# Performance work log

Measured on AMD Instinct MI355X. Metric: run time of the kernel, lower is better.

## Reference

```python
import jax, jax.numpy as jnp
import numpy as np

DIM = 1024
NUM_HEADS = 16
HEAD_DIM = DIM // NUM_HEADS
SCALE = HEAD_DIM ** -0.5


def setup_inputs() -> dict:
    key = jax.random.key(0)
    k1, k2, k3, k4, k5 = jax.random.split(key, 5)
    B, N = 2, 2048
    h = jax.random.normal(k1, (B, N, DIM), dtype=jnp.float32)
    mask = jax.random.uniform(k2, (B, N), dtype=jnp.float32)  # non-negative, sqrt-safe
    # nn.Linear(dim, dim*3, bias=False): weight applied as x @ W^T; store as [dim, 3*dim]
    w_qkv = jax.random.normal(k3, (DIM, 3 * DIM), dtype=jnp.float32) * (DIM ** -0.5)
    w_proj = jax.random.normal(k4, (DIM, DIM), dtype=jnp.float32) * (DIM ** -0.5)
    b_proj = jax.random.normal(k5, (DIM,), dtype=jnp.float32) * 0.01
    return {"h": h, "mask": mask, "w_qkv": w_qkv, "w_proj": w_proj, "b_proj": b_proj}


def reference(h, mask, w_qkv, w_proj, b_proj):
    B, N, C = h.shape
    H, D = NUM_HEADS, HEAD_DIM
    # qkv projection -> [3, B, H, N, D]
    qkv = (h @ w_qkv).reshape(B, N, 3, H, D).transpose(2, 0, 3, 1, 4)
    q, k, v = qkv[0], qkv[1], qkv[2]
    # scores [B,H,N,N]; scale applied to logits (same math as (q@k^T)*scale)
    attn = jax.nn.softmax(jnp.einsum('bhqd,bhkd->bhqk', q, k) * SCALE, axis=-1)
    # post-softmax multiplicative mask over the KEY dimension: mask[B,N]->[B,1,1,N]
    attn = attn * mask[:, None, None, :]
    new_mask = jnp.sqrt(mask)
    out = jnp.einsum('bhqk,bhkd->bhqd', attn, v)          # [B,H,N,D]
    out = out.transpose(0, 2, 1, 3).reshape(B, N, C)       # [B,N,C]
    out = out @ w_proj + b_proj
    return out, new_mask
```

## Files before the change

kernel.cpp:

```cpp
#include <hip/hip_runtime.h>
#include <hip/hip_bf16.h>
#include <math.h>

#define DIMC   1024
#define NHEADS 16
#define HDIM   64
#define BATCH  2
#define SEQ    2048
#define SCALE  0.125f
#define QSCL   (0.125f * 1.44269504088896341f)

typedef unsigned short u16;
typedef unsigned int   u32;
typedef __attribute__((ext_vector_type(8))) short bf16x8;
typedef _Float16 f16x8 __attribute__((ext_vector_type(8)));
typedef __attribute__((ext_vector_type(4))) float f32x4;

#define BHND ((size_t)BATCH * NHEADS * SEQ * HDIM)
#define MROWS ((size_t)BATCH * SEQ)

__device__ __forceinline__ u16 f2bf(float x) {
    __hip_bfloat16 h = __float2bfloat16(x);
    return *reinterpret_cast<u16*>(&h);
}
__device__ __forceinline__ u16 f2h(float x) {
    _Float16 h = (_Float16)x;
    return *reinterpret_cast<u16*>(&h);
}
__device__ __forceinline__ u32 cvt_pk_bf16(float a, float b) {
    u32 r;
    asm("v_cvt_pk_bf16_f32 %0, %1, %2" : "=v"(r) : "v"(a), "v"(b));
    return r;
}
__device__ __forceinline__ void gload_lds16(const u16* g, u16* l) {
    __builtin_amdgcn_global_load_lds(
        (const __attribute__((address_space(1))) unsigned int*)g,
        (__attribute__((address_space(3))) unsigned int*)l, 16, 0, 0);
}

__global__ __launch_bounds__(256) void prep_h_kernel(
    const float* __restrict__ in, u16* __restrict__ outh,
    const float* __restrict__ mask, float* __restrict__ outm)
{
    int bid = blockIdx.x;
    if (bid < 2048) {
        int i = (bid * 256 + threadIdx.x) * 8;
        float4 a = *(const float4*)&in[i];
        float4 b = *(const float4*)&in[i + 4];
        float v[8] = {a.x, a.y, a.z, a.w, b.x, b.y, b.z, b.w};
        bf16x8 o;
        #pragma unroll
        for (int j = 0; j < 8; ++j) o[j] = (short)f2h(v[j]);
        *(bf16x8*)&outh[i] = o;
    } else {
        int i = ((bid - 2048) * 256 + threadIdx.x) * 8;
        float4 a = *(const float4*)&mask[i];
        float4 b = *(const float4*)&mask[i + 4];
        float4 oa = make_float4(sqrtf(a.x), sqrtf(a.y), sqrtf(a.z), sqrtf(a.w));
        float4 ob = make_float4(sqrtf(b.x), sqrtf(b.y), sqrtf(b.z), sqrtf(b.w));
        *(float4*)&outm[i]     = oa;
        *(float4*)&outm[i + 4] = ob;
    }
}

__global__ __launch_bounds__(256) void prep_w_kernel(
    const float* __restrict__ Wq, const float* __restrict__ Wp,
    u16* __restrict__ Tq, u16* __restrict__ Tp)
{
    __shared__ float Ws[64][65];
    const int K = DIMC;
    const float* W; u16* T; int N, nb;
    if (blockIdx.y < 48) { W = Wq; T = Tq; N = 3072; nb = blockIdx.y * 64; }
    else                 { W = Wp; T = Tp; N = 1024; nb = (blockIdx.y - 48) * 64; }
    const int kb  = blockIdx.x * 64;
    const int tid = threadIdx.x;
    const int jr  = (tid & 15) * 4;
    const int ir  = tid >> 4;
    #pragma unroll
    for (int it = 0; it < 4; ++it) {
        int i = ir + it * 16;
        *(float4*)&Ws[i][jr] = *(const float4*)&W[(size_t)(kb + i) * N + nb + jr];
    }
    __syncthreads();
    const int n  = tid >> 2;
    const int k0 = (tid & 3) * 16;
    bf16x8 h0, h1;
    #pragma unroll
    for (int kk = 0; kk < 8; ++kk) {
        h0[kk] = (short)f2h(Ws[k0 + kk][n]);
        h1[kk] = (short)f2h(Ws[k0 + 8 + kk][n]);
    }
    size_t off = (size_t)(nb + n) * K + kb + k0;
    *(bf16x8*)&T[off]     = h0;
    *(bf16x8*)&T[off + 8] = h1;
}

template <int MODE>
__global__ __launch_bounds__(256) void gemm_f16_kernel(
    const u16* __restrict__ A, const u16* __restrict__ B,
    const float* __restrict__ bias, const float* __restrict__ vmask,
    float* __restrict__ outf, u16* __restrict__ outb,
    int M, int N, int K)
{
    __shared__ __align__(16) u16 lds[2][128 * 64];

    const int bm   = blockIdx.y * 128;
    const int bn   = blockIdx.x * 128;
    const int tid  = threadIdx.x;
    const int wid  = tid >> 6;
    const int lane = tid & 63;
    const int lo   = lane & 15;
    const int g4   = lane >> 4;
    const int wr   = wid >> 1, wc = wid & 1;

    const int srow8 = lane >> 3;
    const int scolx = 8 * ((lane & 7) ^ srow8);
    const u16* g0  = (wid < 2)
        ? A + (size_t)(bm + (wid & 1) * 64 + srow8) * K + scolx
        : B + (size_t)(bn + (wid & 1) * 64 + srow8) * K + scolx;
    u16* lbase = &lds[wid >> 1][(wid & 1) * 64 * 64];

    f32x4 acc[4][4] = {};

    for (int k0 = 0; k0 < K; k0 += 64) {
        const u16* g = g0 + k0;
        #pragma unroll
        for (int s = 0; s < 8; ++s)
            gload_lds16(g + (size_t)s * 8 * K, lbase + s * 512);
        __syncthreads();

        #pragma unroll
        for (int ks = 0; ks < 2; ++ks) {
            const int csw = 8 * ((4 * ks + g4) ^ (lo & 7));
            f16x8 bfr[4];
            #pragma unroll
            for (int ni = 0; ni < 4; ++ni)
                bfr[ni] = *(const f16x8*)&lds[1][(wc * 64 + ni * 16 + lo) * 64 + csw];
            #pragma unroll
            for (int mi = 0; mi < 4; ++mi) {
                f16x8 a = *(const f16x8*)&lds[0][(wr * 64 + mi * 16 + lo) * 64 + csw];
                #pragma unroll
                for (int ni = 0; ni < 4; ++ni)
                    acc[mi][ni] = __builtin_amdgcn_mfma_f32_16x16x32_f16(a, bfr[ni], acc[mi][ni], 0, 0, 0);
            }
        }
        __syncthreads();
    }

    if (MODE == 0) {
        #pragma unroll
        for (int mi = 0; mi < 4; ++mi) {
            int m0 = bm + wr * 64 + mi * 16 + 4 * g4;
            #pragma unroll
            for (int ni = 0; ni < 4; ++ni) {
                int n0    = bn + wc * 64 + ni * 16;
                int which = n0 >> 10;
                int head  = (n0 & 1023) >> 6;
                int d     = (n0 & 63) + lo;
                if (which == 0) {
                    #pragma unroll
                    for (int r = 0; r < 4; ++r) {
                        int m = m0 + r, b = m >> 11, seq = m & 2047;
                        outb[(((size_t)b * NHEADS + head) * SEQ + seq) * HDIM + d] =
                            f2bf(acc[mi][ni][r] * QSCL);
                    }
                } else if (which == 1) {
                    #pragma unroll
                    for (int r = 0; r < 4; ++r) {
                        int m = m0 + r, b = m >> 11, seq = m & 2047;
                        outb[BHND + (((size_t)b * NHEADS + head) * SEQ + seq) * HDIM + d] =
                            f2bf(acc[mi][ni][r]);
                    }
                } else {
                    int b = m0 >> 11, seq0 = m0 & 2047;
                    float4 mv = *(const float4*)&vmask[b * SEQ + seq0];
                    ushort4 o;
                    o.x = f2bf(acc[mi][ni][0] * mv.x);
                    o.y = f2bf(acc[mi][ni][1] * mv.y);
                    o.z = f2bf(acc[mi][ni][2] * mv.z);
                    o.w = f2bf(acc[mi][ni][3] * mv.w);
                    *(ushort4*)&outb[2 * BHND +
                        (((size_t)b * NHEADS + head) * HDIM + d) * SEQ + seq0] = o;
                }
            }
        }
    } else {
        #pragma unroll
        for (int ni = 0; ni < 4; ++ni) {
            int col = bn + wc * 64 + ni * 16 + lo;
            float bv = bias[col];
            #pragma unroll
            for (int mi = 0; mi < 4; ++mi) {
                int m0 = bm + wr * 64 + mi * 16 + 4 * g4;
                #pragma unroll
                for (int r = 0; r < 4; ++r)
                    outf[(size_t)(m0 + r) * N + col] = acc[mi][ni][r] + bv;
            }
        }
    }
}

__global__ __launch_bounds__(256) void attn_mfma_kernel(
    const u16* __restrict__ qb, const u16* __restrict__ kb,
    const u16* __restrict__ vtb, u16* __restrict__ oA)
{
    __shared__ __align__(16) u16 Ks[64 * 64];
    __shared__ __align__(16) u16 Vt[64 * 64];
    __shared__ __align__(16) u16 Plds[4][16 * 72];

    const int bid  = blockIdx.x;
    const int qt   = bid & 31;
    const int h    = (bid >> 5) & 15;
    const int b    = bid >> 9;
    const int tid  = threadIdx.x;
    const int wid  = tid >> 6;
    const int lane = tid & 63;
    const int lo   = lane & 15;
    const int g    = lane >> 4;

    const size_t bh = (size_t)b * NHEADS + h;
    const int qbase = qt * 64 + wid * 16;

    const u16* qrowp = qb + (bh * SEQ + qbase + lo) * HDIM + 8 * g;
    const bf16x8 aq0 = *(const bf16x8*)(qrowp);
    const bf16x8 aq1 = *(const bf16x8*)(qrowp + 32);

    const int srow  = tid >> 2;
    const int scol  = (tid & 3) * 16;
    const int swz   = (srow & 7) << 3;
    const int idx0  = srow * 64 + (scol ^ swz);
    const int idx1  = srow * 64 + ((scol + 8) ^ swz);
    const u16* kgp  = kb  + (bh * SEQ  + srow) * HDIM + scol;
    const u16* vgp  = vtb + (bh * HDIM + srow) * SEQ  + scol;

    int kof0[4], kof1[4];
    #pragma unroll
    for (int kt = 0; kt < 4; ++kt) {
        int key  = lo + 16 * kt;
        int kbse = key * 64;
        int ksw  = (key & 7) << 3;
        kof0[kt] = kbse + ((8 * g) ^ ksw);
        kof1[kt] = kbse + ((32 + 8 * g) ^ ksw);
    }
    int vof0[4], vof1[4];
    #pragma unroll
    for (int dt = 0; dt < 4; ++dt) {
        int vbse = (lo + 16 * dt) * 64;
        int vsw  = (lo & 7) << 3;
        vof0[dt] = vbse + ((8 * g) ^ vsw);
        vof1[dt] = vbse + ((32 + 8 * g) ^ vsw);
    }

    bf16x8 ones;
    #pragma unroll
    for (int j = 0; j < 8; ++j) ones[j] = (short)0x3F80;

    f32x4 acc[4] = {};
    f32x4 accl = {};

    u16* pw = &Plds[wid][0];

    bf16x8 rk0 = *(const bf16x8*)(kgp);
    bf16x8 rk1 = *(const bf16x8*)(kgp + 8);
    bf16x8 rv0 = *(const bf16x8*)(vgp);
    bf16x8 rv1 = *(const bf16x8*)(vgp + 8);

    for (int k0 = 0; k0 < SEQ; k0 += 64) {
        __syncthreads();
        *(bf16x8*)&Ks[idx0] = rk0;
        *(bf16x8*)&Ks[idx1] = rk1;
        *(bf16x8*)&Vt[idx0] = rv0;
        *(bf16x8*)&Vt[idx1] = rv1;
        __syncthreads();
        if (k0 + 64 < SEQ) {
            const u16* kn = kgp + (size_t)(k0 + 64) * HDIM;
            rk0 = *(const bf16x8*)(kn);
            rk1 = *(const bf16x8*)(kn + 8);
            rv0 = *(const bf16x8*)(vgp + k0 + 64);
            rv1 = *(const bf16x8*)(vgp + k0 + 64 + 8);
        }

        f32x4 s[4];
        #pragma unroll
        for (int kt = 0; kt < 4; ++kt) {
            f32x4 t = {};
            t = __builtin_amdgcn_mfma_f32_16x16x32_bf16(*(const bf16x8*)&Ks[kof0[kt]], aq0, t, 0, 0, 0);
            t = __builtin_amdgcn_mfma_f32_16x16x32_bf16(*(const bf16x8*)&Ks[kof1[kt]], aq1, t, 0, 0, 0);
            s[kt] = t;
        }

        #pragma unroll
        for (int kt = 0; kt < 4; ++kt) {
            uint2 pr;
            pr.x = cvt_pk_bf16(__builtin_amdgcn_exp2f(s[kt][0]),
                               __builtin_amdgcn_exp2f(s[kt][1]));
            pr.y = cvt_pk_bf16(__builtin_amdgcn_exp2f(s[kt][2]),
                               __builtin_amdgcn_exp2f(s[kt][3]));
            *(uint2*)&pw[lo * 72 + 16 * kt + 4 * g] = pr;
        }

        const bf16x8 pa0 = *(const bf16x8*)&pw[lo * 72 + 8 * g];
        const bf16x8 pa1 = *(const bf16x8*)&pw[lo * 72 + 32 + 8 * g];
        accl = __builtin_amdgcn_mfma_f32_16x16x32_bf16(pa0, ones, accl, 0, 0, 0);
        accl = __builtin_amdgcn_mfma_f32_16x16x32_bf16(pa1, ones, accl, 0, 0, 0);
        #pragma unroll
        for (int dt = 0; dt < 4; ++dt) {
            acc[dt] = __builtin_amdgcn_mfma_f32_16x16x32_bf16(pa0, *(const bf16x8*)&Vt[vof0[dt]], acc[dt], 0, 0, 0);
            acc[dt] = __builtin_amdgcn_mfma_f32_16x16x32_bf16(pa1, *(const bf16x8*)&Vt[vof1[dt]], acc[dt], 0, 0, 0);
        }
    }

    #pragma unroll
    for (int r = 0; r < 4; ++r) {
        float invq = 1.f / accl[r];
        size_t row = (size_t)b * SEQ + qbase + 4 * g + r;
        u16* dst = oA + row * DIMC + h * HDIM + lo;
        #pragma unroll
        for (int dt = 0; dt < 4; ++dt)
            dst[16 * dt] = f2h(acc[dt][r] * invq);
    }
}

extern "C" void kernel_launch(void* const* d_in, const int* in_sizes, int n_in,
                              void* d_out, int out_size, void* d_ws, size_t ws_size,
                              hipStream_t stream)
{
    const float* h      = (const float*)d_in[0];
    const float* mask   = (const float*)d_in[1];
    const float* w_qkv  = (const float*)d_in[2];
    const float* w_proj = (const float*)d_in[3];
    const float* b_proj = (const float*)d_in[4];
    float* out = (float*)d_out;

    u16* qkv = (u16*)d_ws;
    u16* wqT = qkv + 3 * BHND;
    u16* wpT = wqT + (size_t)3072 * 1024;
    u16* hA  = wpT + (size_t)1024 * 1024;
    u16* oA  = hA;

    prep_h_kernel<<<2050, 256, 0, stream>>>(h, hA, mask, out + MROWS * DIMC);
    prep_w_kernel<<<dim3(16, 64), 256, 0, stream>>>(w_qkv, w_proj, wqT, wpT);

    gemm_f16_kernel<0><<<dim3(24, 32), 256, 0, stream>>>(
        hA, wqT, nullptr, mask, nullptr, qkv, MROWS, 3 * DIMC, DIMC);

    attn_mfma_kernel<<<BATCH * NHEADS * (SEQ / 64), 256, 0, stream>>>(
        qkv, qkv + BHND, qkv + 2 * BHND, oA);

    gemm_f16_kernel<1><<<dim3(8, 32), 256, 0, stream>>>(
        oA, wpT, b_proj, nullptr, out, nullptr, MROWS, DIMC, DIMC);
}
```

Before: 128.9 us.

## Split attention key range across two wave groups with LDS reduction

The attention kernel now launches 512 threads per block. The second group of four waves processes the upper half of the key sequence in parallel with the first, so each wave runs 16 key tiles instead of 32. At the end, the second group writes its partial numerators and row sums to shared memory, and the first group adds them before normalizing and storing. This shortens the serial per-block loop and raises waves in flight, at the cost of more LDS per block, an extra reduction with two barriers, and possibly fewer resident blocks per CU.

Result: no change. 128.2 us, median of 2 (-0.6%).

```diff
diff --git a/kernel.cpp b/kernel.cpp
--- a/kernel.cpp
+++ b/kernel.cpp
@@ -200,13 +200,11 @@
     }
 }
 
-__global__ __launch_bounds__(256) void attn_mfma_kernel(
+__global__ __launch_bounds__(512) void attn_mfma_kernel(
     const u16* __restrict__ qb, const u16* __restrict__ kb,
     const u16* __restrict__ vtb, u16* __restrict__ oA)
 {
-    __shared__ __align__(16) u16 Ks[64 * 64];
-    __shared__ __align__(16) u16 Vt[64 * 64];
-    __shared__ __align__(16) u16 Plds[4][16 * 72];
+    __shared__ __align__(16) u16 smem[25600];
 
     const int bid  = blockIdx.x;
     const int qt   = bid & 31;
@@ -217,21 +215,27 @@
     const int lane = tid & 63;
     const int lo   = lane & 15;
     const int g    = lane >> 4;
+    const int qsub = wid & 3;
+    const int kh   = wid >> 2;
 
     const size_t bh = (size_t)b * NHEADS + h;
-    const int qbase = qt * 64 + wid * 16;
+    const int qbase = qt * 64 + qsub * 16;
 
     const u16* qrowp = qb + (bh * SEQ + qbase + lo) * HDIM + 8 * g;
     const bf16x8 aq0 = *(const bf16x8*)(qrowp);
     const bf16x8 aq1 = *(const bf16x8*)(qrowp + 32);
 
-    const int srow  = tid >> 2;
-    const int scol  = (tid & 3) * 16;
+    const int shalf = tid >> 8;
+    const int stid  = tid & 255;
+    const int srow  = stid >> 2;
+    const int scol  = (stid & 3) * 16;
     const int swz   = (srow & 7) << 3;
     const int idx0  = srow * 64 + (scol ^ swz);
     const int idx1  = srow * 64 + ((scol + 8) ^ swz);
-    const u16* kgp  = kb  + (bh * SEQ  + srow) * HDIM + scol;
-    const u16* vgp  = vtb + (bh * HDIM + srow) * SEQ  + scol;
+    u16* ksh = smem + (size_t)shalf * 4096;
+    u16* vsh = smem + 8192 + (size_t)shalf * 4096;
+    const u16* kgp = kb  + (bh * SEQ + (size_t)shalf * 1024 + srow) * HDIM + scol;
+    const u16* vgp = vtb + (bh * HDIM + srow) * SEQ + (size_t)shalf * 1024 + scol;
 
     int kof0[4], kof1[4];
     #pragma unroll
@@ -258,35 +262,38 @@
     f32x4 acc[4] = {};
     f32x4 accl = {};
 
-    u16* pw = &Plds[wid][0];
+    u16* pw = smem + 16384 + (size_t)wid * 1152;
+    const u16* Kc = smem + (size_t)kh * 4096;
+    const u16* Vc = smem + 8192 + (size_t)kh * 4096;
+    const int NT = 16;
 
     bf16x8 rk0 = *(const bf16x8*)(kgp);
     bf16x8 rk1 = *(const bf16x8*)(kgp + 8);
     bf16x8 rv0 = *(const bf16x8*)(vgp);
     bf16x8 rv1 = *(const bf16x8*)(vgp + 8);
 
-    for (int k0 = 0; k0 < SEQ; k0 += 64) {
+    for (int t = 0; t < NT; ++t) {
         __syncthreads();
-        *(bf16x8*)&Ks[idx0] = rk0;
-        *(bf16x8*)&Ks[idx1] = rk1;
-        *(bf16x8*)&Vt[idx0] = rv0;
-        *(bf16x8*)&Vt[idx1] = rv1;
+        *(bf16x8*)&ksh[idx0] = rk0;
+        *(bf16x8*)&ksh[idx1] = rk1;
+        *(bf16x8*)&vsh[idx0] = rv0;
+        *(bf16x8*)&vsh[idx1] = rv1;
         __syncthreads();
-        if (k0 + 64 < SEQ) {
-            const u16* kn = kgp + (size_t)(k0 + 64) * HDIM;
+        if (t + 1 < NT) {
+            const u16* kn = kgp + (size_t)(t + 1) * 64 * HDIM;
             rk0 = *(const bf16x8*)(kn);
             rk1 = *(const bf16x8*)(kn + 8);
-            rv0 = *(const bf16x8*)(vgp + k0 + 64);
-            rv1 = *(const bf16x8*)(vgp + k0 + 64 + 8);
+            rv0 = *(const bf16x8*)(vgp + (t + 1) * 64);
+            rv1 = *(const bf16x8*)(vgp + (t + 1) * 64 + 8);
         }
 
         f32x4 s[4];
         #pragma unroll
         for (int kt = 0; kt < 4; ++kt) {
-            f32x4 t = {};
-            t = __builtin_amdgcn_mfma_f32_16x16x32_bf16(*(const bf16x8*)&Ks[kof0[kt]], aq0, t, 0, 0, 0);
-            t = __builtin_amdgcn_mfma_f32_16x16x32_bf16(*(const bf16x8*)&Ks[kof1[kt]], aq1, t, 0, 0, 0);
-            s[kt] = t;
+            f32x4 t2 = {};
+            t2 = __builtin_amdgcn_mfma_f32_16x16x32_bf16(*(const bf16x8*)&Kc[kof0[kt]], aq0, t2, 0, 0, 0);
+            t2 = __builtin_amdgcn_mfma_f32_16x16x32_bf16(*(const bf16x8*)&Kc[kof1[kt]], aq1, t2, 0, 0, 0);
+            s[kt] = t2;
         }
 
         #pragma unroll
@@ -305,19 +312,36 @@
         accl = __builtin_amdgcn_mfma_f32_16x16x32_bf16(pa1, ones, accl, 0, 0, 0);
         #pragma unroll
         for (int dt = 0; dt < 4; ++dt) {
-            acc[dt] = __builtin_amdgcn_mfma_f32_16x16x32_bf16(pa0, *(const bf16x8*)&Vt[vof0[dt]], acc[dt], 0, 0, 0);
-            acc[dt] = __builtin_amdgcn_mfma_f32_16x16x32_bf16(pa1, *(const bf16x8*)&Vt[vof1[dt]], acc[dt], 0, 0, 0);
-        }
-    }
-
-    #pragma unroll
-    for (int r = 0; r < 4; ++r) {
-        float invq = 1.f / accl[r];
-        size_t row = (size_t)b * SEQ + qbase + 4 * g + r;
-        u16* dst = oA + row * DIMC + h * HDIM + lo;
+            acc[dt] = __builtin_amdgcn_mfma_f32_16x16x32_bf16(pa0, *(const bf16x8*)&Vc[vof0[dt]], acc[dt], 0, 0, 0);
+            acc[dt] = __builtin_amdgcn_mfma_f32_16x16x32_bf16(pa1, *(const bf16x8*)&Vc[vof1[dt]], acc[dt], 0, 0, 0);
+        }
+    }
+
+    __syncthreads();
+    float* Xm = (float*)smem;
+    if (kh == 1) {
+        float* dst = Xm + ((size_t)qsub * 64 + lane) * 21;
         #pragma unroll
         for (int dt = 0; dt < 4; ++dt)
-            dst[16 * dt] = f2h(acc[dt][r] * invq);
+            #pragma unroll
+            for (int r = 0; r < 4; ++r) dst[dt * 4 + r] = acc[dt][r];
+        #pragma unroll
+        for (int r = 0; r < 4; ++r) dst[16 + r] = accl[r];
+    }
+    __syncthreads();
+    if (kh == 0) {
+        const float* src = Xm + ((size_t)qsub * 64 + lane) * 21;
+        #pragma unroll
+        for (int r = 0; r < 4; ++r) accl[r] += src[16 + r];
+        #pragma unroll
+        for (int r = 0; r < 4; ++r) {
+            float invq = 1.f / accl[r];
+            size_t row = (size_t)b * SEQ + qbase + 4 * g + r;
+            u16* dst = oA + row * DIMC + h * HDIM + lo;
+            #pragma unroll
+            for (int dt = 0; dt < 4; ++dt)
+                dst[16 * dt] = f2h((acc[dt][r] + src[dt * 4 + r]) * invq);
+        }
     }
 }
 
@@ -344,7 +368,7 @@
     gemm_f16_kernel<0><<<dim3(24, 32), 256, 0, stream>>>(
         hA, wqT, nullptr, mask, nullptr, qkv, MROWS, 3 * DIMC, DIMC);
 
-    attn_mfma_kernel<<<BATCH * NHEADS * (SEQ / 64), 256, 0, stream>>>(
+    attn_mfma_kernel<<<BATCH * NHEADS * (SEQ / 64), 512, 0, stream>>>(
         qkv, qkv + BHND, qkv + 2 * BHND, oA);
 
     gemm_f16_kernel<1><<<dim3(8, 32), 256, 0, stream>>>(
```
